# Optimization experiments

Measured on AMD Instinct MI355X. Metric: run time of the kernel, lower is better.

Reference implementation:

```python
import jax, jax.numpy as jnp
import numpy as np
import math

H, N2, RANK, CH, LMAX = 256, 64, 1, 1, 2048
DT_MIN, DT_MAX = 1e-3, 1e-1


def setup_inputs() -> dict:
    key = jax.random.key(0)
    kP, kPi, kC, kCi, kdt = jax.random.split(key, 5)
    # DPLR 'lin' init: A = -1/2 - i*pi*n  (real_part=0.5, imag_part=pi*arange(N//2))
    A_real = 0.5 * jnp.ones((H, N2), jnp.float32)
    A_imag = math.pi * jnp.broadcast_to(jnp.arange(N2, dtype=jnp.float32), (H, N2))
    # B_init='constant': B = ones (complex)
    B_real = jnp.ones((H, N2), jnp.float32)
    B_imag = jnp.zeros((H, N2), jnp.float32)
    # P = randn complex (rank, H, N//2); torch complex randn has per-component std 1/sqrt(2)
    s = 1.0 / math.sqrt(2.0)
    P_real = s * jax.random.normal(kP, (RANK, H, N2), jnp.float32)
    P_imag = s * jax.random.normal(kPi, (RANK, H, N2), jnp.float32)
    # C (output projection) randn complex (channels, H, N//2)
    C_real = s * jax.random.normal(kC, (CH, H, N2), jnp.float32)
    C_imag = s * jax.random.normal(kCi, (CH, H, N2), jnp.float32)
    # dt log-uniform in [dt_min, dt_max]
    log_dt = math.log(DT_MIN) + jax.random.uniform(kdt, (H,), jnp.float32) * (
        math.log(DT_MAX) - math.log(DT_MIN))
    return {
        "A_real": A_real, "A_imag": A_imag,
        "B_real": B_real, "B_imag": B_imag,
        "P_real": P_real, "P_imag": P_imag,
        "C_real": C_real, "C_imag": C_imag,
        "log_dt": log_dt, "L": LMAX,
    }


def _krylov_doubling(dA, dB, L):
    """Matrix-power doubling scan (mirrors `power`): columns [dB, dA dB, ..., dA^{L-1} dB].

    dA: (H, N, N) complex, dB: (H, N) complex -> (H, N, L) complex.
    """
    x = dB[..., None]  # (H, N, 1)
    Ap = dA
    while x.shape[-1] < L:
        x = jnp.concatenate([x, Ap @ x], axis=-1)  # doubling step
        Ap = Ap @ Ap  # repeated squaring, as in power()
    return x[..., :L]


def reference(A_real, A_imag, B_real, B_imag, P_real, P_imag, C_real, C_imag, log_dt, L):
    # Build DPLR state matrix: A = diag(Lambda) - P P^*
    Lam = (-A_real - 1j * A_imag).astype(jnp.complex64)        # (H, N2)
    P = (P_real + 1j * P_imag).astype(jnp.complex64)           # (R, H, N2)
    B = (B_real + 1j * B_imag).astype(jnp.complex64)           # (H, N2)
    C = (C_real + 1j * C_imag).astype(jnp.complex64)           # (CH, H, N2)
    n2 = Lam.shape[-1]
    I = jnp.eye(n2, dtype=jnp.complex64)
    A_mat = Lam[:, :, None] * I - jnp.einsum('rhn,rhm->hnm', P, jnp.conj(P))  # (H,N2,N2)
    dt = jnp.exp(log_dt).astype(jnp.complex64)                 # (H,)
    # Bilinear (Tustin) discretization: dA = (I - dt/2 A)^{-1}(I + dt/2 A), dB = (I - dt/2 A)^{-1} dt B
    half = 0.5 * dt[:, None, None] * A_mat
    M_bwd = I - half
    dA = jnp.linalg.solve(M_bwd, I + half)                     # (H,N2,N2)
    dB = jnp.linalg.solve(M_bwd, (dt[:, None] * B)[..., None])[..., 0]  # (H,N2)
    # Kernel via power-doubling Krylov scan, then project: K[c,h,l] = 2 Re(C dA^l dB)
    x = _krylov_doubling(dA, dB, L)                            # (H,N2,L)
    K = 2.0 * jnp.real(jnp.einsum('chn,hnl->chl', C, x))       # (CH,H,L)
    return K
```

## Files before the change

kernel.cpp:

```cpp
#include <hip/hip_runtime.h>


#define LL 2048

struct C2 { float re, im; };

__device__ __forceinline__ C2 cmul(C2 a, C2 b){ return {a.re*b.re - a.im*b.im, a.re*b.im + a.im*b.re}; }
__device__ __forceinline__ C2 cadd(C2 a, C2 b){ return {a.re+b.re, a.im+b.im}; }
__device__ __forceinline__ C2 csub(C2 a, C2 b){ return {a.re-b.re, a.im-b.im}; }
__device__ __forceinline__ C2 cinv(C2 a){ float s=1.0f/(a.re*a.re+a.im*a.im); return {a.re*s, -a.im*s}; }
__device__ __forceinline__ C2 cscale(float s, C2 a){ return {s*a.re, s*a.im}; }
__device__ __forceinline__ C2 ld2(float2 v){ return {v.x, v.y}; }
__device__ __forceinline__ float2 st2(C2 v){ return make_float2(v.re, v.im); }

template<int CTRL>
__device__ __forceinline__ float dpp_add(float x){
  int t = __builtin_amdgcn_update_dpp(0, __float_as_int(x), CTRL, 0xF, 0xF, true);
  return x + __int_as_float(t);
}
__device__ __forceinline__ float wave_sum63(float x){
  x = dpp_add<0xB1>(x);
  x = dpp_add<0x4E>(x);
  x = dpp_add<0x124>(x);
  x = dpp_add<0x128>(x);
  x = dpp_add<0x142>(x);
  x = dpp_add<0x143>(x);
  return x;
}
__device__ __forceinline__ float bcast63(float x){
  return __int_as_float(__builtin_amdgcn_readlane(__float_as_int(x), 63));
}
__device__ __forceinline__ float rdlane(float v, int l){
  return __int_as_float(__builtin_amdgcn_readlane(__float_as_int(v), l));
}
__device__ __forceinline__ float shr1(float x){
  return __int_as_float(__builtin_amdgcn_update_dpp(0, __float_as_int(x), 0x138, 0xF, 0xF, true));
}

__device__ __forceinline__ void tri_solve64(const C2 wl, C2 va, const int lane,
                                            float& so_re, float& so_im)
{
    C2 wsh = { shr1(wl.re), shr1(wl.im) };
    const float w0r = rdlane(wl.re, 0);
    const float w0i = rdlane(wl.im, 0);
    so_re = 0.0f; so_im = 0.0f;
    for (int j = 0; j < 64; j += 2) {
        const float s0r = rdlane(va.re, j);
        const float s0i = rdlane(va.im, j);
        const float v1r = rdlane(va.re, j + 1);
        const float v1i = rdlane(va.im, j + 1);
        const float s1r = v1r + (w0r*s0r - w0i*s0i);
        const float s1i = v1i + (w0r*s0i + w0i*s0r);
        if (lane == j)     { so_re = s0r; so_im = s0i; }
        if (lane == j + 1) { so_re = s1r; so_im = s1i; }
        const C2 wsh1 = { shr1(wsh.re), shr1(wsh.im) };
        va.re += wsh.re*s0r - wsh.im*s0i;
        va.im += wsh.re*s0i + wsh.im*s0r;
        va.re += wsh1.re*s1r - wsh1.im*s1i;
        va.im += wsh1.re*s1i + wsh1.im*s1r;
        wsh.re = shr1(wsh1.re);
        wsh.im = shr1(wsh1.im);
    }
}

__global__ __launch_bounds__(512)
__attribute__((amdgpu_waves_per_eu(2, 2)))
void ssm_dplr_kernel(
    const float* __restrict__ A_real, const float* __restrict__ A_imag,
    const float* __restrict__ B_real, const float* __restrict__ B_imag,
    const float* __restrict__ P_real, const float* __restrict__ P_imag,
    const float* __restrict__ C_real, const float* __restrict__ C_imag,
    const float* __restrict__ log_dt, float* __restrict__ out)
{
    const int h    = blockIdx.x;
    const int t    = threadIdx.x;
    const int lane = t & 63;
    const int wid  = t >> 6;

    extern __shared__ char sm[];
    float2* Abuf = (float2*)sm;
    float2* Cs   = (float2*)(sm + 32768);
    float2* tw   = Cs;
    float2* ta   = Cs + 512;
    float2* gA   = (float2*)(sm + 49152);
    float2* qA   = gA + 64;
    float2* g64A = gA + 128;
    float2* TgA  = gA + 192;
    float2* TpA  = gA + 256;
    float2* rqA  = gA + 320;
    float2* rxA  = gA + 384;
    float2* wvA  = gA + 448;
    float2* avA  = gA + 512;

    const int idx = h * 64 + lane;
    const float dt = expf(log_dt[h]);
    const float c  = 0.5f * dt;

    const C2 lam = { -A_real[idx], -A_imag[idx] };
    const C2 p   = {  P_real[idx],  P_imag[idx] };
    const C2 Bv  = {  B_real[idx],  B_imag[idx] };
    const C2 Cv  = {  C_real[idx],  C_imag[idx] };
    const C2 pc  = { p.re, -p.im };

    const C2 d = cinv(C2{ 1.0f - c*lam.re, -c*lam.im });
    const C2 g = cmul(d, C2{ 1.0f + c*lam.re, c*lam.im });

    C2 sv = cscale(p.re*p.re + p.im*p.im, d);
    C2 uv = cmul(cmul(d, pc), Bv);
    sv.re = bcast63(wave_sum63(sv.re)); sv.im = bcast63(wave_sum63(sv.im));
    uv.re = bcast63(wave_sum63(uv.re)); uv.im = bcast63(wave_sum63(uv.im));

    const C2 beta  = cscale(c, cinv(C2{ 1.0f + c*sv.re, c*sv.im }));
    const C2 bs    = cmul(beta, sv);
    const C2 gamma = { -c*(1.0f - bs.re), c*bs.im };

    const C2 q  = cmul(d, p);
    const C2 r  = cmul(pc, csub(gamma, cmul(beta, g)));
    const C2 x0 = cscale(dt, csub(cmul(d, Bv), cmul(cmul(beta, uv), q)));

    const C2 g2  = cmul(g,  g);
    const C2 g4  = cmul(g2, g2);
    const C2 g8  = cmul(g4, g4);
    const C2 g16 = cmul(g8, g8);
    const C2 g32 = cmul(g16,g16);
    const C2 g64 = cmul(g32,g32);

    if (wid == 0) {
        gA[lane]   = st2(g);
        qA[lane]   = st2(q);
        g64A[lane] = st2(g64);
        rqA[lane]  = st2(cmul(r, q));
        rxA[lane]  = st2(cmul(r, x0));
    }
    __syncthreads();

    {
        C2 cur = {1.0f, 0.0f};
        if (wid & 1) cur = g8;
        if (wid & 2) cur = cmul(cur, g16);
        if (wid & 4) cur = cmul(cur, g32);
        #pragma unroll
        for (int jj = 0; jj < 8; ++jj) {
            const int j = 8*wid + jj;
            Abuf[j*64 + ((lane + j) & 63)] = st2(cur);
            cur = cmul(cur, g);
        }
    }
    __syncthreads();

    {
        C2 accw = {0,0}, acca = {0,0};
        #pragma unroll
        for (int kk = 0; kk < 8; ++kk) {
            const int n = 8*wid + kk;
            const C2 Gv = ld2(Abuf[lane*64 + ((n + lane) & 63)]);
            const C2 fq = ld2(rqA[n]);
            const C2 fx = ld2(rxA[n]);
            accw = cadd(accw, cmul(Gv, fq));
            acca = cadd(acca, cmul(Gv, fx));
        }
        tw[wid*64 + lane] = st2(accw);
        ta[wid*64 + lane] = st2(acca);
    }
    __syncthreads();
    if (t < 64) {
        C2 sw = {0,0}, sa = {0,0};
        #pragma unroll
        for (int w2 = 0; w2 < 8; ++w2) {
            sw = cadd(sw, ld2(tw[w2*64 + t]));
            sa = cadd(sa, ld2(ta[w2*64 + t]));
        }
        wvA[t] = st2(sw);
        avA[t] = st2(sa);
    }
    __syncthreads();

    C2 Mk[64];
    if (wid == 0) {
        const C2 wl = ld2(wvA[lane]);
        float tau_re, tau_im;
        tri_solve64(wl, wl, lane, tau_re, tau_im);
        C2 pp = { rdlane(tau_re, 0), rdlane(tau_im, 0) };
        C2 dd = {0,0};
        for (int i = 1; i <= 62; ++i) {
            const C2 ti = { rdlane(tau_re, i), rdlane(tau_im, i) };
            dd = cadd(cmul(dd, g), pp);
            pp = cadd(cmul(pp, g), ti);
        }
        TgA[lane] = st2(cmul(g, pp));
        TpA[lane] = st2(cadd(pp, cmul(g, dd)));
    } else if (wid == 1) {
        const C2 wl = ld2(wvA[lane]);
        float sg_re, sg_im;
        tri_solve64(wl, ld2(avA[lane]), lane, sg_re, sg_im);
        C2 x = x0;
        for (int j = 0; j < 64; ++j) {
            Abuf[j*64 + ((lane + j) & 63)] = st2(x);
            const float sjr = rdlane(sg_re, j);
            const float sji = rdlane(sg_im, j);
            const float nr = g.re*x.re - g.im*x.im + sjr*q.re - sji*q.im;
            const float ni = g.re*x.im + g.im*x.re + sjr*q.im + sji*q.re;
            x.re = nr; x.im = ni;
        }
    } else if (wid == 2) {
        #pragma unroll
        for (int k = 0; k < 64; ++k) {
            const C2 gn = ld2(gA[k]);
            Mk[k] = cinv(csub(gn, g));
        }
    }
    __syncthreads();

    if (wid == 2) {
        const C2 Tgm = ld2(TgA[lane]);
        const C2 Tp  = ld2(TpA[lane]);
        const C2 g63 = cmul(g64, cinv(g));
        const C2 S   = cmul(r, cadd(cscale(64.0f, g63), Tp));
        const C2 diagv = cadd(g64, cmul(q, S));
        #pragma unroll
        for (int k = 0; k < 64; ++k) {
            const C2 qn   = ld2(qA[k]);
            const C2 g64n = ld2(g64A[k]);
            const C2 Tgn  = ld2(TgA[k]);
            const C2 num  = cmul(r, cadd(csub(g64n, g64), csub(Tgn, Tgm)));
            const C2 off  = cmul(cmul(qn, num), Mk[k]);
            const bool isd = (lane == k);
            Mk[k].re = isd ? diagv.re : off.re;
            Mk[k].im = isd ? diagv.im : off.im;
        }
        C2 Ci = Cv;
        Cs[lane] = st2(Ci);
        for (int i = 1; i < 32; ++i) {
            float ar0 = 0.0f, ai0 = 0.0f, ar1 = 0.0f, ai1 = 0.0f;
            #pragma unroll
            for (int k = 0; k < 64; k += 2) {
                const float c0r = rdlane(Ci.re, k);
                const float c0i = rdlane(Ci.im, k);
                const float c1r = rdlane(Ci.re, k + 1);
                const float c1i = rdlane(Ci.im, k + 1);
                ar0 += c0r*Mk[k].re   - c0i*Mk[k].im;
                ai0 += c0r*Mk[k].im   + c0i*Mk[k].re;
                ar1 += c1r*Mk[k+1].re - c1i*Mk[k+1].im;
                ai1 += c1r*Mk[k+1].im + c1i*Mk[k+1].re;
            }
            Ci.re = ar0 + ar1;
            Ci.im = ai0 + ai1;
            Cs[i*64 + lane] = st2(Ci);
        }
    }
    __syncthreads();

    {
        float accK[4] = {0.0f, 0.0f, 0.0f, 0.0f};
        #pragma unroll 8
        for (int n = 0; n < 64; ++n) {
            const float2 xv = Abuf[lane*64 + ((n + lane) & 63)];
            #pragma unroll
            for (int rr = 0; rr < 4; ++rr) {
                const float2 cv = Cs[(4*wid + rr)*64 + n];
                accK[rr] += cv.x*xv.x - cv.y*xv.y;
            }
        }
        float* outh = out + h * LL;
        #pragma unroll
        for (int rr = 0; rr < 4; ++rr) {
            outh[(4*wid + rr)*64 + lane] = 2.0f * accK[rr];
        }
    }
}

extern "C" void kernel_launch(void* const* d_in, const int* in_sizes, int n_in,
                              void* d_out, int out_size, void* d_ws, size_t ws_size,
                              hipStream_t stream) {
    const float* A_real = (const float*)d_in[0];
    const float* A_imag = (const float*)d_in[1];
    const float* B_real = (const float*)d_in[2];
    const float* B_imag = (const float*)d_in[3];
    const float* P_real = (const float*)d_in[4];
    const float* P_imag = (const float*)d_in[5];
    const float* C_real = (const float*)d_in[6];
    const float* C_imag = (const float*)d_in[7];
    const float* log_dt = (const float*)d_in[8];
    float* out = (float*)d_out;

    const size_t lds = 49152 + 9*64*sizeof(float2);
    ssm_dplr_kernel<<<256, 512, lds, stream>>>(
        A_real, A_imag, B_real, B_imag, P_real, P_imag,
        C_real, C_imag, log_dt, out);
}
```

Baseline: 114.4 us.

## Build projection matrix across all waves in LDS and serialize C-power and Krylov phases

Building the 64x64 matrix M used to step C through its powers is now split across all 8 waves. Each wave computes 8 columns and writes them to LDS, reusing the Abuf region, instead of wave 2 holding all 64 complex entries in registers. The C power iteration then reads M from LDS as float4, and the current C vector is broadcast through a small LDS buffer instead of readlane. The cost is that the x-recurrence in wave 1 now runs after the C iteration rather than alongside it, adding two extra barriers and serializing two phases that previously overlapped.

Result: slower. 134.8 us (+17.9%).

```diff
diff --git a/kernel.cpp b/kernel.cpp
--- a/kernel.cpp
+++ b/kernel.cpp
@@ -79,6 +79,7 @@
 
     extern __shared__ char sm[];
     float2* Abuf = (float2*)sm;
+    float4* Ml4  = (float4*)sm;
     float2* Cs   = (float2*)(sm + 32768);
     float2* tw   = Cs;
     float2* ta   = Cs + 512;
@@ -91,6 +92,7 @@
     float2* rxA  = gA + 384;
     float2* wvA  = gA + 448;
     float2* avA  = gA + 512;
+    float2* cbuf = gA + 576;
 
     const int idx = h * 64 + lane;
     const float dt = expf(log_dt[h]);
@@ -175,7 +177,12 @@
     }
     __syncthreads();
 
-    C2 Mk[64];
+    C2 idmk[8];
+    #pragma unroll
+    for (int kk = 0; kk < 8; ++kk) {
+        idmk[kk] = cinv(csub(ld2(gA[8*wid + kk]), g));
+    }
+    float sg_re = 0.0f, sg_im = 0.0f;
     if (wid == 0) {
         const C2 wl = ld2(wvA[lane]);
         float tau_re, tau_im;
@@ -191,8 +198,68 @@
         TpA[lane] = st2(cadd(pp, cmul(g, dd)));
     } else if (wid == 1) {
         const C2 wl = ld2(wvA[lane]);
-        float sg_re, sg_im;
         tri_solve64(wl, ld2(avA[lane]), lane, sg_re, sg_im);
+    }
+    __syncthreads();
+
+    {
+        const C2 Tgm = ld2(TgA[lane]);
+        const C2 Tp  = ld2(TpA[lane]);
+        const C2 g63 = cmul(g64, cinv(g));
+        const C2 S   = cmul(r, cadd(cscale(64.0f, g63), Tp));
+        const C2 diagv = cadd(g64, cmul(q, S));
+        #pragma unroll
+        for (int kp = 0; kp < 4; ++kp) {
+            C2 v0, v1;
+            #pragma unroll
+            for (int u = 0; u < 2; ++u) {
+                const int kk = 2*kp + u;
+                const int k  = 8*wid + kk;
+                const C2 qn   = ld2(qA[k]);
+                const C2 g64n = ld2(g64A[k]);
+                const C2 Tgn  = ld2(TgA[k]);
+                const C2 num  = cmul(r, cadd(csub(g64n, g64), csub(Tgn, Tgm)));
+                const C2 off  = cmul(cmul(qn, num), idmk[kk]);
+                const bool isd = (lane == k);
+                C2 v;
+                v.re = isd ? diagv.re : off.re;
+                v.im = isd ? diagv.im : off.im;
+                if (u == 0) v0 = v; else v1 = v;
+            }
+            Ml4[(4*wid + kp)*64 + lane] = make_float4(v0.re, v0.im, v1.re, v1.im);
+        }
+    }
+    __syncthreads();
+
+    if (wid == 2) {
+        C2 Ci = Cv;
+        Cs[lane]   = st2(Ci);
+        cbuf[lane] = st2(Ci);
+        const float4* cb4 = (const float4*)cbuf;
+        for (int i = 1; i < 32; ++i) {
+            float ar0 = 0.0f, ai0 = 0.0f, ar1 = 0.0f, ai1 = 0.0f;
+            #pragma unroll 1
+            for (int k2b = 0; k2b < 32; k2b += 8) {
+                #pragma unroll
+                for (int kk = 0; kk < 8; ++kk) {
+                    const int k2 = k2b + kk;
+                    const float4 mm = Ml4[k2*64 + lane];
+                    const float4 cc = cb4[k2];
+                    ar0 += cc.x*mm.x - cc.y*mm.y;
+                    ai0 += cc.x*mm.y + cc.y*mm.x;
+                    ar1 += cc.z*mm.z - cc.w*mm.w;
+                    ai1 += cc.z*mm.w + cc.w*mm.z;
+                }
+            }
+            Ci.re = ar0 + ar1;
+            Ci.im = ai0 + ai1;
+            cbuf[lane]      = st2(Ci);
+            Cs[i*64 + lane] = st2(Ci);
+        }
+    }
+    __syncthreads();
+
+    if (wid == 1) {
         C2 x = x0;
         for (int j = 0; j < 64; ++j) {
             Abuf[j*64 + ((lane + j) & 63)] = st2(x);
@@ -201,51 +268,6 @@
             const float nr = g.re*x.re - g.im*x.im + sjr*q.re - sji*q.im;
             const float ni = g.re*x.im + g.im*x.re + sjr*q.im + sji*q.re;
             x.re = nr; x.im = ni;
-        }
-    } else if (wid == 2) {
-        #pragma unroll
-        for (int k = 0; k < 64; ++k) {
-            const C2 gn = ld2(gA[k]);
-            Mk[k] = cinv(csub(gn, g));
-        }
-    }
-    __syncthreads();
-
-    if (wid == 2) {
-        const C2 Tgm = ld2(TgA[lane]);
-        const C2 Tp  = ld2(TpA[lane]);
-        const C2 g63 = cmul(g64, cinv(g));
-        const C2 S   = cmul(r, cadd(cscale(64.0f, g63), Tp));
-        const C2 diagv = cadd(g64, cmul(q, S));
-        #pragma unroll
-        for (int k = 0; k < 64; ++k) {
-            const C2 qn   = ld2(qA[k]);
-            const C2 g64n = ld2(g64A[k]);
-            const C2 Tgn  = ld2(TgA[k]);
-            const C2 num  = cmul(r, cadd(csub(g64n, g64), csub(Tgn, Tgm)));
-            const C2 off  = cmul(cmul(qn, num), Mk[k]);
-            const bool isd = (lane == k);
-            Mk[k].re = isd ? diagv.re : off.re;
-            Mk[k].im = isd ? diagv.im : off.im;
-        }
-        C2 Ci = Cv;
-        Cs[lane] = st2(Ci);
-        for (int i = 1; i < 32; ++i) {
-            float ar0 = 0.0f, ai0 = 0.0f, ar1 = 0.0f, ai1 = 0.0f;
-            #pragma unroll
-            for (int k = 0; k < 64; k += 2) {
-                const float c0r = rdlane(Ci.re, k);
-                const float c0i = rdlane(Ci.im, k);
-                const float c1r = rdlane(Ci.re, k + 1);
-                const float c1i = rdlane(Ci.im, k + 1);
-                ar0 += c0r*Mk[k].re   - c0i*Mk[k].im;
-                ai0 += c0r*Mk[k].im   + c0i*Mk[k].re;
-                ar1 += c1r*Mk[k+1].re - c1i*Mk[k+1].im;
-                ai1 += c1r*Mk[k+1].im + c1i*Mk[k+1].re;
-            }
-            Ci.re = ar0 + ar1;
-            Ci.im = ai0 + ai1;
-            Cs[i*64 + lane] = st2(Ci);
         }
     }
     __syncthreads();
@@ -283,7 +305,7 @@
     const float* log_dt = (const float*)d_in[8];
     float* out = (float*)d_out;
 
-    const size_t lds = 49152 + 9*64*sizeof(float2);
+    const size_t lds = 49152 + 10*64*sizeof(float2);
     ssm_dplr_kernel<<<256, 512, lds, stream>>>(
         A_real, A_imag, B_real, B_imag, P_real, P_imag,
         C_real, C_imag, log_dt, out);
```
